# Optimization experiments

Measured on AMD Instinct MI355X. Metric: run time of the kernel, lower is better.

The kernel has to match this reference:

```python
import jax, jax.numpy as jnp
import numpy as np

N = 8388608          # number of samples (2**23)
T_MAX = 100000       # number of distinct time values -> ~84 ties per time


def setup_inputs() -> dict:
    key = jax.random.key(0)
    k1, k2, k3 = jax.random.split(key, 3)
    inp = jax.random.normal(k1, (N,), dtype=jnp.float32)            # log hazards
    target = jax.random.randint(k2, (N,), 0, T_MAX, dtype=jnp.int32)  # times
    weight = jax.random.randint(k3, (N,), 0, 2, dtype=jnp.int32)      # event indicator
    return {"input": inp, "target": target, "weight": weight}


def _cox_efron_npll(log_hz, time, event):
    """Negative Cox partial log-likelihood with Efron tie correction, mean reduction.

    Faithful to torchsurv's _partial_likelihood_efron: per unique time j,
    pll_j = sum_{i in H_j} log_hz_i - sum_{l=0}^{m_j-1} log(D_j - (l/m_j)*T_j)
    where H_j = events at time j, D_j = sum of exp(log_hz) over risk set (t>=t_j),
    T_j = sum of exp(log_hz) over H_j, m_j = |H_j|; loss = -mean over j with m_j>0.
    """
    n = log_hz.shape[0]
    order = jnp.argsort(time)                       # sort by time (group-sum math is tie-order invariant)
    t = time[order]
    lh = log_hz[order]
    ev = event[order].astype(lh.dtype)

    # group id per sample: 0..(num_unique-1), padded groups beyond that are empty
    new_grp = jnp.concatenate([jnp.zeros((1,), jnp.int32), (t[1:] != t[:-1]).astype(jnp.int32)])
    seg = jnp.cumsum(new_grp)                       # [n] int32

    hz = jnp.exp(lh)
    grp_hz = jax.ops.segment_sum(hz, seg, num_segments=n)          # sum exp per time group
    denom_naive = jnp.cumsum(grp_hz[::-1])[::-1]                   # risk-set sums (suffix over groups)
    m = jax.ops.segment_sum(ev, seg, num_segments=n)               # events per group
    log_nom = jax.ops.segment_sum(lh * ev, seg, num_segments=n)    # sum of log_hz over H_j
    ties = jax.ops.segment_sum(hz * ev, seg, num_segments=n)       # sum of exp over H_j

    # rank l in [0, m_j) of each event within its group
    csum_e = jnp.cumsum(ev)
    events_before = jnp.concatenate([jnp.zeros((1,), lh.dtype), jnp.cumsum(m)[:-1]])
    rank = csum_e - 1.0 - events_before[seg]
    mg = jnp.maximum(m[seg], 1.0)
    term = jnp.where(ev > 0.0,
                     jnp.log(denom_naive[seg] - (rank / mg) * ties[seg]),
                     0.0)
    log_denom = jax.ops.segment_sum(term, seg, num_segments=n)

    include = (m > 0.0).astype(lh.dtype)
    pll = jnp.where(m > 0.0, log_nom - log_denom, 0.0)
    # reduction='mean': -pll.nanmean() over groups that contain events
    return -(jnp.sum(pll) / jnp.sum(include))


def reference(input, target, weight):
    return _cox_efron_npll(input, target, weight)
```

## Files before the change

### kernel.cpp

```cpp
#include <hip/hip_runtime.h>

#define TMAXV 100000
#define CHUNK 256
#define NCHUNK ((TMAXV + CHUNK - 1) / CHUNK)
#define WB 256
#define LOGWB 8
#define SB ((TMAXV + WB - 1) / WB)
#define SBP 512
#define TILE 4096
#define RPT 16
#define KS 8
#define CAP 4096
#define RPH (CAP / 256)


__device__ __forceinline__ float block_reduce_sum(float v, float* sdata) {
    int lane = threadIdx.x & 63;
    int wid  = threadIdx.x >> 6;
    #pragma unroll
    for (int off = 32; off > 0; off >>= 1)
        v += __shfl_down(v, off, 64);
    if (lane == 0) sdata[wid] = v;
    __syncthreads();
    if (wid == 0) {
        v = (lane < 4) ? sdata[lane] : 0.0f;
        v += __shfl_down(v, 2, 64);
        v += __shfl_down(v, 1, 64);
    }
    return v;
}


__global__ void count_pfx_kernel(const int* __restrict__ tgt,
                                 int* __restrict__ pfx_arr,
                                 int* __restrict__ cnt_t, int n) {
    __shared__ int lc[SBP];
    __shared__ int ls[SBP];
    int tid = threadIdx.x, tile = blockIdx.x;
    lc[tid] = 0; lc[tid + 256] = 0;
    __syncthreads();
    int lo = tile * TILE, hi = min(n, lo + TILE);
    for (int i = lo + tid; i < hi; i += 256)
        atomicAdd(&lc[tgt[i] >> LOGWB], 1);
    __syncthreads();
    int c0 = lc[tid], c1 = lc[tid + 256];
    int i1 = tid + 256;
    ls[tid] = c0; ls[i1] = c1;
    __syncthreads();
    for (int off = 1; off < SBP; off <<= 1) {
        int a0 = (tid >= off) ? ls[tid - off] : 0;
        int a1 = (i1  >= off) ? ls[i1  - off] : 0;
        __syncthreads();
        ls[tid] += a0; ls[i1] += a1;
        __syncthreads();
    }
    size_t rb = (size_t)tile * SBP;
    pfx_arr[rb + tid] = ls[tid] - c0;
    pfx_arr[rb + i1]  = ls[i1]  - c1;
    cnt_t[rb + tid] = c0;
    cnt_t[rb + i1]  = c1;
}

__global__ void transpose_kernel(const int* __restrict__ A,
                                 int* __restrict__ B, int rows, int cols) {
    __shared__ int tl[32][33];
    int bx = blockIdx.x * 32, by = blockIdx.y * 32;
    int x = threadIdx.x, y = threadIdx.y;
    #pragma unroll
    for (int j = 0; j < 32; j += 8)
        if (by + y + j < rows && bx + x < cols)
            tl[y + j][x] = A[(size_t)(by + y + j) * cols + bx + x];
    __syncthreads();
    #pragma unroll
    for (int j = 0; j < 32; j += 8)
        if (bx + y + j < cols && by + x < rows)
            B[(size_t)(bx + y + j) * rows + by + x] = tl[x][y + j];
}

__global__ void tile_scan_kernel(int* __restrict__ cnt_s,
                                 int* __restrict__ totals, int nt) {
    __shared__ int ls[256];
    int s = blockIdx.x, tid = threadIdx.x;
    int run = 0;
    for (int t0 = 0; t0 < nt; t0 += 256) {
        int t = t0 + tid;
        int c = (t < nt) ? cnt_s[(size_t)s * nt + t] : 0;
        ls[tid] = c;
        __syncthreads();
        for (int off = 1; off < 256; off <<= 1) {
            int a = (tid >= off) ? ls[tid - off] : 0;
            __syncthreads();
            ls[tid] += a;
            __syncthreads();
        }
        int incl = ls[tid];
        int tot  = ls[255];
        if (t < nt) cnt_s[(size_t)s * nt + t] = run + incl - c;
        run += tot;
        __syncthreads();
    }
    if (tid == 0) totals[s] = run;
}

__global__ void bucket_base_kernel(const int* __restrict__ totals,
                                   int* __restrict__ base, int n) {
    __shared__ int ls[SBP];
    int tid = threadIdx.x;
    int c = totals[tid];
    ls[tid] = c;
    __syncthreads();
    for (int off = 1; off < SBP; off <<= 1) {
        int a = (tid >= off) ? ls[tid - off] : 0;
        __syncthreads();
        ls[tid] += a;
        __syncthreads();
    }
    base[tid] = ls[tid] - c;
    if (tid == 0) base[SBP] = n;
}

__global__ void scatter_kernel(const float* __restrict__ lh,
                               const int*   __restrict__ tgt,
                               const int*   __restrict__ ev,
                               const int*   __restrict__ pfx_arr,
                               const int*   __restrict__ tilebase_t,
                               const int*   __restrict__ base,
                               unsigned* __restrict__ val,
                               double* __restrict__ acc, int n) {
    __shared__ uint2 fd[TILE];
    __shared__ int pfx[SBP];
    __shared__ int tb[SBP];
    __shared__ int lrank[SBP];
    __shared__ float sdata[4];
    int tid  = threadIdx.x;
    int tile = blockIdx.x;
    int lo   = tile * TILE;
    int cnt_here = min(TILE, n - lo);
    int i1 = tid + 256;
    size_t rb = (size_t)tile * SBP;

    pfx[tid] = pfx_arr[rb + tid];
    pfx[i1]  = pfx_arr[rb + i1];
    tb[tid]  = base[tid] + tilebase_t[rb + tid];
    tb[i1]   = base[i1]  + tilebase_t[rb + i1];
    lrank[tid] = 0; lrank[i1] = 0;

    unsigned rbits[RPT];
    int      rk[RPT];
    float xl = 0.f;
    if (lo + TILE <= n) {
        const int4*   tgt4 = (const int4*)(tgt + lo);
        const int4*   ev4  = (const int4*)(ev + lo);
        const float4* lh4  = (const float4*)(lh + lo);
        #pragma unroll
        for (int q = 0; q < RPT / 4; ++q) {
            int idx = q * 256 + tid;
            int4   t4 = tgt4[idx];
            int4   e4 = ev4[idx];
            float4 x4 = lh4[idx];
            int   tv[4] = {t4.x, t4.y, t4.z, t4.w};
            int   evv[4] = {e4.x, e4.y, e4.z, e4.w};
            float xv[4] = {x4.x, x4.y, x4.z, x4.w};
            #pragma unroll
            for (int j = 0; j < 4; ++j) {
                int k = q * 4 + j;
                int e = evv[j] & 1;
                float x = xv[j];
                float h = __expf(x);
                rbits[k] = (__float_as_uint(h) & 0x7FFFFF00u)
                         | (unsigned)(tv[j] & (WB - 1))
                         | ((unsigned)e << 31);
                rk[k] = tv[j] >> LOGWB;
                if (e) xl += x;
            }
        }
    } else {
        #pragma unroll
        for (int k = 0; k < RPT; ++k) {
            int i = lo + k * 256 + tid;
            if (i < n) {
                int t = tgt[i];
                int e = ev[i] & 1;
                float x = lh[i];
                float h = __expf(x);
                rbits[k] = (__float_as_uint(h) & 0x7FFFFF00u)
                         | (unsigned)(t & (WB - 1))
                         | ((unsigned)e << 31);
                rk[k] = t >> LOGWB;
                if (e) xl += x;
            } else {
                rk[k] = -1;
            }
        }
    }
    __syncthreads();

    #pragma unroll
    for (int k = 0; k < RPT; ++k) {
        if (rk[k] >= 0) {
            int b = rk[k];
            int r = atomicAdd(&lrank[b], 1);
            fd[pfx[b] + r] = make_uint2(rbits[k], (unsigned)(tb[b] + r));
        }
    }
    __syncthreads();

    for (int p = tid; p < cnt_here; p += 256) {
        uint2 r2 = fd[p];
        val[r2.y] = r2.x;
    }

    float rl = block_reduce_sum(xl, sdata);
    if (tid == 0) atomicAdd(&acc[2], (double)rl);
}

__global__ void bucket_hist_kernel(const unsigned* __restrict__ val,
                                   const int* __restrict__ base,
                                   float* __restrict__ partials,
                                   float* __restrict__ chunk_sum) {
    __shared__ unsigned fv[CAP];
    __shared__ unsigned cnt[WB];
    __shared__ unsigned rankc[WB];
    __shared__ unsigned pfx[WB];
    __shared__ unsigned ls[WB];
    __shared__ float sdata[4];
    int tid = threadIdx.x;
    int b   = blockIdx.x >> 3;
    int k   = blockIdx.x & (KS - 1);
    int lo0 = base[b], len = base[b + 1] - lo0;
    int lo  = lo0 + (int)(((long long)len * k) / KS);
    int hi  = lo0 + (int)(((long long)len * (k + 1)) / KS);

    float sh = 0.f, cm = 0.f, th = 0.f;

    for (int c0 = lo; c0 < hi; c0 += CAP) {
        int c1 = min(hi, c0 + CAP);
        cnt[tid] = 0; rankc[tid] = 0;
        __syncthreads();

        unsigned rv[RPH];
        int      rs[RPH];
        #pragma unroll
        for (int u = 0; u < RPH; ++u) {
            int i = c0 + u * 256 + tid;
            if (i < c1) {
                rv[u] = val[i];
                rs[u] = (int)(rv[u] & (WB - 1));
                atomicAdd(&cnt[rs[u]], 1u);
            } else {
                rs[u] = -1;
            }
        }
        __syncthreads();

        unsigned c = cnt[tid];
        ls[tid] = c;
        __syncthreads();
        for (int off = 1; off < 256; off <<= 1) {
            unsigned a = (tid >= off) ? ls[tid - off] : 0u;
            __syncthreads();
            ls[tid] += a;
            __syncthreads();
        }
        pfx[tid] = ls[tid] - c;
        __syncthreads();

        #pragma unroll
        for (int u = 0; u < RPH; ++u) {
            if (rs[u] >= 0) {
                unsigned r = atomicAdd(&rankc[rs[u]], 1u);
                fv[pfx[rs[u]] + r] = rv[u];
            }
        }
        __syncthreads();

        int s0 = (int)pfx[tid], e0 = s0 + (int)cnt[tid];
        for (int p = s0; p < e0; ++p) {
            unsigned bits = fv[p];
            float h = fabsf(__uint_as_float(bits));
            sh += h;
            if (bits >> 31) { cm += 1.0f; th += h; }
        }
        __syncthreads();
    }

    float* pbase = partials + (size_t)blockIdx.x * 3 * WB;
    pbase[0 * WB + tid] = sh;
    pbase[1 * WB + tid] = cm;
    pbase[2 * WB + tid] = th;

    float st = block_reduce_sum(sh, sdata);
    if (tid == 0) unsafeAtomicAdd(&chunk_sum[b], st);
}

__global__ void chunk_scan_kernel(const float* __restrict__ chunk_sum,
                                  double* __restrict__ chunk_off) {
    __shared__ double ds[512];
    int tid = threadIdx.x;
    double own = (tid < NCHUNK) ? (double)chunk_sum[tid] : 0.0;
    ds[tid] = own;
    __syncthreads();
    for (int off = 1; off < 512; off <<= 1) {
        double add = (tid + off < 512) ? ds[tid + off] : 0.0;
        __syncthreads();
        ds[tid] += add;
        __syncthreads();
    }
    if (tid < NCHUNK) chunk_off[tid] = ds[tid] - own;
}

__global__ void pll_suffix_kernel(const float* __restrict__ partials,
                                  const double* __restrict__ chunk_off,
                                  double* __restrict__ acc) {
    __shared__ float sf[CHUNK];
    __shared__ float sdata[4];
    __shared__ float sdata2[4];
    int tid = threadIdx.x;
    int b   = blockIdx.x;
    float sh = 0.f, cm = 0.f, th = 0.f;
    #pragma unroll
    for (int k = 0; k < KS; ++k) {
        const float* pbase = partials + (size_t)(b * KS + k) * 3 * WB;
        sh += pbase[0 * WB + tid];
        cm += pbase[1 * WB + tid];
        th += pbase[2 * WB + tid];
    }
    sf[tid] = sh;
    __syncthreads();
    for (int off = 1; off < CHUNK; off <<= 1) {
        float add = (tid + off < CHUNK) ? sf[tid + off] : 0.0f;
        __syncthreads();
        sf[tid] += add;
        __syncthreads();
    }
    int t = b * CHUNK + tid;
    float pll = 0.0f, inc = 0.0f;
    if (t < TMAXV && cm > 0.5f) {
        float D    = (float)(chunk_off[b] + (double)sf[tid]);
        int   mi   = (int)(cm + 0.5f);
        float step = th / cm;
        float s = 0.0f;
        for (int l = 0; l < mi; ++l)
            s += __logf(D - (float)l * step);
        pll = -s;
        inc = 1.0f;
    }
    float rp = block_reduce_sum(pll, sdata);
    __syncthreads();
    float ri = block_reduce_sum(inc, sdata2);
    if (threadIdx.x == 0) {
        atomicAdd(&acc[0], (double)rp);
        atomicAdd(&acc[1], (double)ri);
    }
}

__global__ void finalize_kernel(const double* __restrict__ acc,
                                float* __restrict__ out) {
    double cnt = acc[1];
    out[0] = (cnt > 0.0) ? (float)(-(acc[0] + acc[2]) / cnt) : 0.0f;
}

__global__ void hist_kernel(const float* __restrict__ lh,
                            const int*   __restrict__ tgt,
                            const int*   __restrict__ ev,
                            float* __restrict__ sum_hz,
                            float* __restrict__ mcnt,
                            float* __restrict__ log_nom,
                            float* __restrict__ ties,
                            int n) {
    int i = blockIdx.x * blockDim.x + threadIdx.x;
    if (i >= n) return;
    float x = lh[i];
    int   t = tgt[i];
    int   e = ev[i];
    float h = __expf(x);
    unsafeAtomicAdd(&sum_hz[t], h);
    if (e) {
        unsafeAtomicAdd(&mcnt[t], 1.0f);
        unsafeAtomicAdd(&log_nom[t], x);
        unsafeAtomicAdd(&ties[t], h);
    }
}

__global__ void chunk_sum_kernel(const float* __restrict__ sum_hz,
                                 float* __restrict__ chunk_sum) {
    __shared__ float sdata[4];
    int i = blockIdx.x * CHUNK + threadIdx.x;
    float v = (i < TMAXV) ? sum_hz[i] : 0.0f;
    v = block_reduce_sum(v, sdata);
    if (threadIdx.x == 0) chunk_sum[blockIdx.x] = v;
}

__global__ void pll_kernel(const float* __restrict__ mcnt,
                           const float* __restrict__ log_nom,
                           const float* __restrict__ ties,
                           const float* __restrict__ sum_hz,
                           const double* __restrict__ chunk_off,
                           double* __restrict__ acc) {
    __shared__ float sf[CHUNK];
    __shared__ float sdata[4];
    __shared__ float sdata2[4];
    int tid = threadIdx.x;
    int t   = blockIdx.x * CHUNK + tid;
    float v = (t < TMAXV) ? sum_hz[t] : 0.0f;
    sf[tid] = v;
    __syncthreads();
    for (int off = 1; off < CHUNK; off <<= 1) {
        float add = (tid + off < CHUNK) ? sf[tid + off] : 0.0f;
        __syncthreads();
        sf[tid] += add;
        __syncthreads();
    }
    float pll = 0.0f, inc = 0.0f;
    if (t < TMAXV) {
        float mv = mcnt[t];
        if (mv > 0.5f) {
            float D    = (float)(chunk_off[blockIdx.x] + (double)sf[tid]);
            float T    = ties[t];
            int   mi   = (int)(mv + 0.5f);
            float step = T / mv;
            float s = 0.0f;
            for (int l = 0; l < mi; ++l)
                s += __logf(D - (float)l * step);
            pll = log_nom[t] - s;
            inc = 1.0f;
        }
    }
    float rp = block_reduce_sum(pll, sdata);
    __syncthreads();
    float ri = block_reduce_sum(inc, sdata2);
    if (threadIdx.x == 0) {
        atomicAdd(&acc[0], (double)rp);
        atomicAdd(&acc[1], (double)ri);
    }
}

extern "C" void kernel_launch(void* const* d_in, const int* in_sizes, int n_in,
                              void* d_out, int out_size, void* d_ws, size_t ws_size,
                              hipStream_t stream) {
    const float* lh  = (const float*)d_in[0];
    const int*   tgt = (const int*)d_in[1];
    const int*   ev  = (const int*)d_in[2];
    float*       out = (float*)d_out;
    int n  = in_sizes[0];
    int nt = (n + TILE - 1) / TILE;

    char* ws = (char*)d_ws;
    size_t off = 0;
    auto take = [&](size_t bytes, size_t align) {
        off = (off + align - 1) & ~(align - 1);
        size_t r = off; off += bytes; return r;
    };
    size_t o_acc    = take(32, 16);
    size_t o_csum   = take((size_t)SBP * 4, 16);
    size_t zero_bytes = off;
    size_t o_base   = take((size_t)(SBP + 1) * 4, 16);
    size_t o_totals = take((size_t)SBP * 4, 16);
    size_t o_coff   = take((size_t)NCHUNK * 8, 16);
    size_t o_pfx    = take((size_t)nt * SBP * 4, 16);
    size_t o_cntt   = take((size_t)nt * SBP * 4, 16);
    size_t o_cnts   = take((size_t)nt * SBP * 4, 16);
    size_t o_val    = take((size_t)n * 4, 16);
    size_t need     = off;
    size_t part_sz  = (size_t)SB * KS * 3 * WB * 4;
    size_t o_part   = o_pfx;
    if (o_part + part_sz > need) need = o_part + part_sz;

    if (ws_size >= need) {
        double*   acc       = (double*)(ws + o_acc);
        float*    chunk_sum = (float*)(ws + o_csum);
        int*      base      = (int*)(ws + o_base);
        int*      totals    = (int*)(ws + o_totals);
        double*   chunk_off = (double*)(ws + o_coff);
        int*      pfx_arr   = (int*)(ws + o_pfx);
        int*      cnt_t     = (int*)(ws + o_cntt);
        int*      cnt_s     = (int*)(ws + o_cnts);
        unsigned* val       = (unsigned*)(ws + o_val);
        float*    partials  = (float*)(ws + o_part);

        hipMemsetAsync(d_ws, 0, zero_bytes, stream);

        count_pfx_kernel<<<nt, 256, 0, stream>>>(tgt, pfx_arr, cnt_t, n);
        transpose_kernel<<<dim3(SBP / 32, (nt + 31) / 32), dim3(32, 8), 0, stream>>>(
            cnt_t, cnt_s, nt, SBP);
        tile_scan_kernel<<<SBP, 256, 0, stream>>>(cnt_s, totals, nt);
        bucket_base_kernel<<<1, SBP, 0, stream>>>(totals, base, n);
        transpose_kernel<<<dim3((nt + 31) / 32, SBP / 32), dim3(32, 8), 0, stream>>>(
            cnt_s, cnt_t, SBP, nt);
        scatter_kernel<<<nt, 256, 0, stream>>>(lh, tgt, ev, pfx_arr, cnt_t, base, val, acc, n);
        bucket_hist_kernel<<<SB * KS, 256, 0, stream>>>(val, base, partials, chunk_sum);
        chunk_scan_kernel<<<1, 512, 0, stream>>>(chunk_sum, chunk_off);
        pll_suffix_kernel<<<NCHUNK, 256, 0, stream>>>(partials, chunk_off, acc);
        finalize_kernel<<<1, 1, 0, stream>>>(acc, out);
    } else {
        size_t f = 0;
        auto ftake = [&](size_t bytes, size_t align) {
            f = (f + align - 1) & ~(align - 1);
            size_t r = f; f += bytes; return r;
        };
        size_t f_acc  = ftake(32, 16);
        size_t f_sum  = ftake((size_t)TMAXV * 4, 16);
        size_t f_m    = ftake((size_t)TMAXV * 4, 16);
        size_t f_ln   = ftake((size_t)TMAXV * 4, 16);
        size_t f_ties = ftake((size_t)TMAXV * 4, 16);
        size_t zb     = f;
        size_t f_csum = ftake((size_t)NCHUNK * 4, 16);
        size_t f_coff = ftake((size_t)NCHUNK * 8, 8);

        double* acc     = (double*)(ws + f_acc);
        float*  sum_hz  = (float*)(ws + f_sum);
        float*  mcnt    = (float*)(ws + f_m);
        float*  log_nom = (float*)(ws + f_ln);
        float*  ties    = (float*)(ws + f_ties);
        float*  chunk_sum = (float*)(ws + f_csum);
        double* chunk_off = (double*)(ws + f_coff);

        hipMemsetAsync(d_ws, 0, zb, stream);

        hist_kernel<<<(n + 255) / 256, 256, 0, stream>>>(lh, tgt, ev, sum_hz, mcnt, log_nom, ties, n);
        chunk_sum_kernel<<<NCHUNK, 256, 0, stream>>>(sum_hz, chunk_sum);
        chunk_scan_kernel<<<1, 512, 0, stream>>>(chunk_sum, chunk_off);
        pll_kernel<<<NCHUNK, 256, 0, stream>>>(mcnt, log_nom, ties, sum_hz, chunk_off, acc);
        finalize_kernel<<<1, 1, 0, stream>>>(acc, out);
    }
}
```

Measured before the change: 228.6 us.

## Move record encoding into count kernel and shrink scatter shared buffer

The count pass now also computes the packed exp/time/event records, writes them to a workspace array, and accumulates the event log-hazard sum. The scatter pass then reads only the precomputed bits and targets. The scatter's shared staging buffer is split into a 4-byte record plus a 2-byte bucket id, and destinations are recomputed at write time, to cut LDS usage. The trade-off is an extra full-size global write and read of the encoded array, plus a larger workspace requirement; a fallback path keeps the old behaviour when the workspace is too small.

```diff
diff --git a/kernel.cpp b/kernel.cpp
--- a/kernel.cpp
+++ b/kernel.cpp
@@ -30,6 +30,13 @@
     return v;
 }
 
+__device__ __forceinline__ unsigned encode_rec(float x, int t, int e) {
+    float h = __expf(x);
+    return (__float_as_uint(h) & 0x7FFFFF00u)
+         | (unsigned)(t & (WB - 1))
+         | ((unsigned)e << 31);
+}
+
 
 __global__ void count_pfx_kernel(const int* __restrict__ tgt,
                                  int* __restrict__ pfx_arr,
@@ -59,6 +66,75 @@
     pfx_arr[rb + i1]  = ls[i1]  - c1;
     cnt_t[rb + tid] = c0;
     cnt_t[rb + i1]  = c1;
+}
+
+__global__ void count_encode_kernel(const int* __restrict__ tgt,
+                                    const float* __restrict__ lh,
+                                    const int* __restrict__ ev,
+                                    int* __restrict__ pfx_arr,
+                                    int* __restrict__ cnt_t,
+                                    unsigned* __restrict__ bitsArr,
+                                    double* __restrict__ acc, int n) {
+    __shared__ int lc[SBP];
+    __shared__ int ls[SBP];
+    __shared__ float sdata[4];
+    int tid = threadIdx.x, tile = blockIdx.x;
+    lc[tid] = 0; lc[tid + 256] = 0;
+    __syncthreads();
+    int lo = tile * TILE;
+    float xl = 0.f;
+    if (lo + TILE <= n) {
+        const int4*   tgt4 = (const int4*)(tgt + lo);
+        const int4*   ev4  = (const int4*)(ev + lo);
+        const float4* lh4  = (const float4*)(lh + lo);
+        uint4* b4 = (uint4*)(bitsArr + lo);
+        #pragma unroll
+        for (int q = 0; q < RPT / 4; ++q) {
+            int idx = q * 256 + tid;
+            int4   t4 = tgt4[idx];
+            int4   e4 = ev4[idx];
+            float4 x4 = lh4[idx];
+            uint4 o;
+            o.x = encode_rec(x4.x, t4.x, e4.x & 1); if (e4.x & 1) xl += x4.x;
+            o.y = encode_rec(x4.y, t4.y, e4.y & 1); if (e4.y & 1) xl += x4.y;
+            o.z = encode_rec(x4.z, t4.z, e4.z & 1); if (e4.z & 1) xl += x4.z;
+            o.w = encode_rec(x4.w, t4.w, e4.w & 1); if (e4.w & 1) xl += x4.w;
+            b4[idx] = o;
+            atomicAdd(&lc[t4.x >> LOGWB], 1);
+            atomicAdd(&lc[t4.y >> LOGWB], 1);
+            atomicAdd(&lc[t4.z >> LOGWB], 1);
+            atomicAdd(&lc[t4.w >> LOGWB], 1);
+        }
+    } else {
+        int hi = min(n, lo + TILE);
+        for (int i = lo + tid; i < hi; i += 256) {
+            int t = tgt[i];
+            int e = ev[i] & 1;
+            float x = lh[i];
+            bitsArr[i] = encode_rec(x, t, e);
+            if (e) xl += x;
+            atomicAdd(&lc[t >> LOGWB], 1);
+        }
+    }
+    __syncthreads();
+    int c0 = lc[tid], c1 = lc[tid + 256];
+    int i1 = tid + 256;
+    ls[tid] = c0; ls[i1] = c1;
+    __syncthreads();
+    for (int off = 1; off < SBP; off <<= 1) {
+        int a0 = (tid >= off) ? ls[tid - off] : 0;
+        int a1 = (i1  >= off) ? ls[i1  - off] : 0;
+        __syncthreads();
+        ls[tid] += a0; ls[i1] += a1;
+        __syncthreads();
+    }
+    size_t rb = (size_t)tile * SBP;
+    pfx_arr[rb + tid] = ls[tid] - c0;
+    pfx_arr[rb + i1]  = ls[i1]  - c1;
+    cnt_t[rb + tid] = c0;
+    cnt_t[rb + i1]  = c1;
+    float rl = block_reduce_sum(xl, sdata);
+    if (tid == 0) atomicAdd(&acc[2], (double)rl);
 }
 
 __global__ void transpose_kernel(const int* __restrict__ A,
@@ -122,12 +198,14 @@
 __global__ void scatter_kernel(const float* __restrict__ lh,
                                const int*   __restrict__ tgt,
                                const int*   __restrict__ ev,
+                               const unsigned* __restrict__ bitsArr,
                                const int*   __restrict__ pfx_arr,
                                const int*   __restrict__ tilebase_t,
                                const int*   __restrict__ base,
                                unsigned* __restrict__ val,
-                               double* __restrict__ acc, int n) {
-    __shared__ uint2 fd[TILE];
+                               double* __restrict__ acc, int n, int fused) {
+    __shared__ unsigned fu[TILE];
+    __shared__ unsigned short bidv[TILE];
     __shared__ int pfx[SBP];
     __shared__ int tb[SBP];
     __shared__ int lrank[SBP];
@@ -148,48 +226,54 @@
     unsigned rbits[RPT];
     int      rk[RPT];
     float xl = 0.f;
-    if (lo + TILE <= n) {
-        const int4*   tgt4 = (const int4*)(tgt + lo);
-        const int4*   ev4  = (const int4*)(ev + lo);
-        const float4* lh4  = (const float4*)(lh + lo);
-        #pragma unroll
-        for (int q = 0; q < RPT / 4; ++q) {
-            int idx = q * 256 + tid;
-            int4   t4 = tgt4[idx];
-            int4   e4 = ev4[idx];
-            float4 x4 = lh4[idx];
-            int   tv[4] = {t4.x, t4.y, t4.z, t4.w};
-            int   evv[4] = {e4.x, e4.y, e4.z, e4.w};
-            float xv[4] = {x4.x, x4.y, x4.z, x4.w};
+    if (fused) {
+        if (lo + TILE <= n) {
+            const uint4* b4  = (const uint4*)(bitsArr + lo);
+            const int4*  tg4 = (const int4*)(tgt + lo);
             #pragma unroll
-            for (int j = 0; j < 4; ++j) {
-                int k = q * 4 + j;
-                int e = evv[j] & 1;
-                float x = xv[j];
-                float h = __expf(x);
-                rbits[k] = (__float_as_uint(h) & 0x7FFFFF00u)
-                         | (unsigned)(tv[j] & (WB - 1))
-                         | ((unsigned)e << 31);
-                rk[k] = tv[j] >> LOGWB;
-                if (e) xl += x;
+            for (int q = 0; q < RPT / 4; ++q) {
+                int idx = q * 256 + tid;
+                uint4 bb = b4[idx];
+                int4  t4 = tg4[idx];
+                rbits[q*4+0] = bb.x; rk[q*4+0] = t4.x >> LOGWB;
+                rbits[q*4+1] = bb.y; rk[q*4+1] = t4.y >> LOGWB;
+                rbits[q*4+2] = bb.z; rk[q*4+2] = t4.z >> LOGWB;
+                rbits[q*4+3] = bb.w; rk[q*4+3] = t4.w >> LOGWB;
             }
+        } else {
+            #pragma unroll
+            for (int k = 0; k < RPT; ++k) {
+                int i = lo + k * 256 + tid;
+                if (i < n) { rbits[k] = bitsArr[i]; rk[k] = tgt[i] >> LOGWB; }
+                else rk[k] = -1;
+            }
         }
     } else {
-        #pragma unroll
-        for (int k = 0; k < RPT; ++k) {
-            int i = lo + k * 256 + tid;
-            if (i < n) {
-                int t = tgt[i];
-                int e = ev[i] & 1;
-                float x = lh[i];
-                float h = __expf(x);
-                rbits[k] = (__float_as_uint(h) & 0x7FFFFF00u)
-                         | (unsigned)(t & (WB - 1))
-                         | ((unsigned)e << 31);
-                rk[k] = t >> LOGWB;
-                if (e) xl += x;
-            } else {
-                rk[k] = -1;
+        if (lo + TILE <= n) {
+            const int4*   tgt4 = (const int4*)(tgt + lo);
+            const int4*   ev4  = (const int4*)(ev + lo);
+            const float4* lh4  = (const float4*)(lh + lo);
+            #pragma unroll
+            for (int q = 0; q < RPT / 4; ++q) {
+                int idx = q * 256 + tid;
+                int4   t4 = tgt4[idx];
+                int4   e4 = ev4[idx];
+                float4 x4 = lh4[idx];
+                rbits[q*4+0] = encode_rec(x4.x, t4.x, e4.x & 1); rk[q*4+0] = t4.x >> LOGWB; if (e4.x & 1) xl += x4.x;
+                rbits[q*4+1] = encode_rec(x4.y, t4.y, e4.y & 1); rk[q*4+1] = t4.y >> LOGWB; if (e4.y & 1) xl += x4.y;
+                rbits[q*4+2] = encode_rec(x4.z, t4.z, e4.z & 1); rk[q*4+2] = t4.z >> LOGWB; if (e4.z & 1) xl += x4.z;
+                rbits[q*4+3] = encode_rec(x4.w, t4.w, e4.w & 1); rk[q*4+3] = t4.w >> LOGWB; if (e4.w & 1) xl += x4.w;
+            }
+        } else {
+            #pragma unroll
+            for (int k = 0; k < RPT; ++k) {
+                int i = lo + k * 256 + tid;
+                if (i < n) {
+                    int t = tgt[i]; int e = ev[i] & 1; float x = lh[i];
+                    rbits[k] = encode_rec(x, t, e);
+                    rk[k] = t >> LOGWB;
+                    if (e) xl += x;
+                } else rk[k] = -1;
             }
         }
     }
@@ -200,18 +284,35 @@
         if (rk[k] >= 0) {
             int b = rk[k];
             int r = atomicAdd(&lrank[b], 1);
-            fd[pfx[b] + r] = make_uint2(rbits[k], (unsigned)(tb[b] + r));
-        }
-    }
-    __syncthreads();
-
-    for (int p = tid; p < cnt_here; p += 256) {
-        uint2 r2 = fd[p];
-        val[r2.y] = r2.x;
-    }
-
-    float rl = block_reduce_sum(xl, sdata);
-    if (tid == 0) atomicAdd(&acc[2], (double)rl);
+            int pos = pfx[b] + r;
+            fu[pos]   = rbits[k];
+            bidv[pos] = (unsigned short)b;
+        }
+    }
+    __syncthreads();
+
+    int pairs = cnt_here >> 1;
+    const uint2* fu2 = (const uint2*)fu;
+    const unsigned* bid2 = (const unsigned*)bidv;
+    for (int q = tid; q < pairs; q += 256) {
+        uint2 bb = fu2[q];
+        unsigned bp = bid2[q];
+        int b0 = (int)(bp & 0xFFFFu);
+        int b1 = (int)(bp >> 16);
+        int p0 = q * 2;
+        val[tb[b0] + (p0     - pfx[b0])] = bb.x;
+        val[tb[b1] + (p0 + 1 - pfx[b1])] = bb.y;
+    }
+    if ((cnt_here & 1) && tid == 0) {
+        int p = cnt_here - 1;
+        int b = (int)bidv[p];
+        val[tb[b] + (p - pfx[b])] = fu[p];
+    }
+
+    if (!fused) {
+        float rl = block_reduce_sum(xl, sdata);
+        if (tid == 0) atomicAdd(&acc[2], (double)rl);
+    }
 }
 
 __global__ void bucket_hist_kernel(const unsigned* __restrict__ val,
@@ -461,12 +562,16 @@
     size_t o_cntt   = take((size_t)nt * SBP * 4, 16);
     size_t o_cnts   = take((size_t)nt * SBP * 4, 16);
     size_t o_val    = take((size_t)n * 4, 16);
-    size_t need     = off;
+    size_t need_med = off;
+    size_t o_bits   = take((size_t)n * 4, 16);
+    size_t need_pri = off;
     size_t part_sz  = (size_t)SB * KS * 3 * WB * 4;
     size_t o_part   = o_pfx;
-    if (o_part + part_sz > need) need = o_part + part_sz;
-
-    if (ws_size >= need) {
+    if (o_part + part_sz > need_med) need_med = o_part + part_sz;
+    if (o_part + part_sz > need_pri) need_pri = o_part + part_sz;
+
+    if (ws_size >= need_med) {
+        int fused = (ws_size >= need_pri) ? 1 : 0;
         double*   acc       = (double*)(ws + o_acc);
         float*    chunk_sum = (float*)(ws + o_csum);
         int*      base      = (int*)(ws + o_base);
@@ -476,18 +581,23 @@
         int*      cnt_t     = (int*)(ws + o_cntt);
         int*      cnt_s     = (int*)(ws + o_cnts);
         unsigned* val       = (unsigned*)(ws + o_val);
+        unsigned* bitsArr   = (unsigned*)(ws + o_bits);
         float*    partials  = (float*)(ws + o_part);
 
         hipMemsetAsync(d_ws, 0, zero_bytes, stream);
 
-        count_pfx_kernel<<<nt, 256, 0, stream>>>(tgt, pfx_arr, cnt_t, n);
+        if (fused)
+            count_encode_kernel<<<nt, 256, 0, stream>>>(tgt, lh, ev, pfx_arr, cnt_t, bitsArr, acc, n);
+        else
+            count_pfx_kernel<<<nt, 256, 0, stream>>>(tgt, pfx_arr, cnt_t, n);
         transpose_kernel<<<dim3(SBP / 32, (nt + 31) / 32), dim3(32, 8), 0, stream>>>(
             cnt_t, cnt_s, nt, SBP);
         tile_scan_kernel<<<SBP, 256, 0, stream>>>(cnt_s, totals, nt);
         bucket_base_kernel<<<1, SBP, 0, stream>>>(totals, base, n);
         transpose_kernel<<<dim3((nt + 31) / 32, SBP / 32), dim3(32, 8), 0, stream>>>(
             cnt_s, cnt_t, SBP, nt);
-        scatter_kernel<<<nt, 256, 0, stream>>>(lh, tgt, ev, pfx_arr, cnt_t, base, val, acc, n);
+        scatter_kernel<<<nt, 256, 0, stream>>>(lh, tgt, ev, bitsArr, pfx_arr, cnt_t, base,
+                                               val, acc, n, fused);
         bucket_hist_kernel<<<SB * KS, 256, 0, stream>>>(val, base, partials, chunk_sum);
         chunk_scan_kernel<<<1, 512, 0, stream>>>(chunk_sum, chunk_off);
         pll_suffix_kernel<<<NCHUNK, 256, 0, stream>>>(partials, chunk_off, acc);
```

New measurement: 233.0 us. No clear change (+1.9%).

## Drop transpose and chunk-scan kernels, fold scans into consumers, slim scatter staging

Applied to the files above, without the earlier changes.

Removes both transpose launches by having the tile scan read the tile-major count matrix with strided loads, and having the scatter kernel read tile bases strided. It also drops the chunk_scan launch: each pll_suffix block now recomputes its own suffix offset by summing the later chunk sums in double. The scatter kernel stages a 4-byte record plus a 16-bit bucket id instead of an 8-byte pair, recomputing destinations from shared tables. count_pfx gets vectorised int4 loads. The aim is fewer launches and less global traffic, at the cost of uncoalesced strided reads and redundant per-block reduction work.

```diff
diff --git a/kernel.cpp b/kernel.cpp
--- a/kernel.cpp
+++ b/kernel.cpp
@@ -30,6 +30,29 @@
     return v;
 }
 
+__device__ __forceinline__ double block_reduce_sum_d(double v, double* sdata) {
+    int lane = threadIdx.x & 63;
+    int wid  = threadIdx.x >> 6;
+    #pragma unroll
+    for (int off = 32; off > 0; off >>= 1)
+        v += __shfl_down(v, off, 64);
+    if (lane == 0) sdata[wid] = v;
+    __syncthreads();
+    if (wid == 0) {
+        v = (lane < 4) ? sdata[lane] : 0.0;
+        v += __shfl_down(v, 2, 64);
+        v += __shfl_down(v, 1, 64);
+    }
+    return v;
+}
+
+__device__ __forceinline__ unsigned encode_rec(float x, int t, int e) {
+    float h = __expf(x);
+    return (__float_as_uint(h) & 0x7FFFFF00u)
+         | (unsigned)(t & (WB - 1))
+         | ((unsigned)e << 31);
+}
+
 
 __global__ void count_pfx_kernel(const int* __restrict__ tgt,
                                  int* __restrict__ pfx_arr,
@@ -39,9 +62,22 @@
     int tid = threadIdx.x, tile = blockIdx.x;
     lc[tid] = 0; lc[tid + 256] = 0;
     __syncthreads();
-    int lo = tile * TILE, hi = min(n, lo + TILE);
-    for (int i = lo + tid; i < hi; i += 256)
-        atomicAdd(&lc[tgt[i] >> LOGWB], 1);
+    int lo = tile * TILE;
+    if (lo + TILE <= n) {
+        const int4* tgt4 = (const int4*)(tgt + lo);
+        #pragma unroll
+        for (int q = 0; q < RPT / 4; ++q) {
+            int4 t4 = tgt4[q * 256 + tid];
+            atomicAdd(&lc[t4.x >> LOGWB], 1);
+            atomicAdd(&lc[t4.y >> LOGWB], 1);
+            atomicAdd(&lc[t4.z >> LOGWB], 1);
+            atomicAdd(&lc[t4.w >> LOGWB], 1);
+        }
+    } else {
+        int hi = min(n, lo + TILE);
+        for (int i = lo + tid; i < hi; i += 256)
+            atomicAdd(&lc[tgt[i] >> LOGWB], 1);
+    }
     __syncthreads();
     int c0 = lc[tid], c1 = lc[tid + 256];
     int i1 = tid + 256;
@@ -61,30 +97,15 @@
     cnt_t[rb + i1]  = c1;
 }
 
-__global__ void transpose_kernel(const int* __restrict__ A,
-                                 int* __restrict__ B, int rows, int cols) {
-    __shared__ int tl[32][33];
-    int bx = blockIdx.x * 32, by = blockIdx.y * 32;
-    int x = threadIdx.x, y = threadIdx.y;
-    #pragma unroll
-    for (int j = 0; j < 32; j += 8)
-        if (by + y + j < rows && bx + x < cols)
-            tl[y + j][x] = A[(size_t)(by + y + j) * cols + bx + x];
-    __syncthreads();
-    #pragma unroll
-    for (int j = 0; j < 32; j += 8)
-        if (bx + y + j < cols && by + x < rows)
-            B[(size_t)(bx + y + j) * rows + by + x] = tl[x][y + j];
-}
-
-__global__ void tile_scan_kernel(int* __restrict__ cnt_s,
-                                 int* __restrict__ totals, int nt) {
+__global__ void tile_scan_direct_kernel(const int* __restrict__ cnt_t,
+                                        int* __restrict__ tilebase_s,
+                                        int* __restrict__ totals, int nt) {
     __shared__ int ls[256];
     int s = blockIdx.x, tid = threadIdx.x;
     int run = 0;
     for (int t0 = 0; t0 < nt; t0 += 256) {
         int t = t0 + tid;
-        int c = (t < nt) ? cnt_s[(size_t)s * nt + t] : 0;
+        int c = (t < nt) ? cnt_t[(size_t)t * SBP + s] : 0;
         ls[tid] = c;
         __syncthreads();
         for (int off = 1; off < 256; off <<= 1) {
@@ -95,7 +116,7 @@
         }
         int incl = ls[tid];
         int tot  = ls[255];
-        if (t < nt) cnt_s[(size_t)s * nt + t] = run + incl - c;
+        if (t < nt) tilebase_s[(size_t)s * nt + t] = run + incl - c;
         run += tot;
         __syncthreads();
     }
@@ -123,11 +144,12 @@
                                const int*   __restrict__ tgt,
                                const int*   __restrict__ ev,
                                const int*   __restrict__ pfx_arr,
-                               const int*   __restrict__ tilebase_t,
+                               const int*   __restrict__ tilebase_s,
                                const int*   __restrict__ base,
                                unsigned* __restrict__ val,
-                               double* __restrict__ acc, int n) {
-    __shared__ uint2 fd[TILE];
+                               double* __restrict__ acc, int n, int nt) {
+    __shared__ unsigned fu[TILE];
+    __shared__ unsigned short bidv[TILE];
     __shared__ int pfx[SBP];
     __shared__ int tb[SBP];
     __shared__ int lrank[SBP];
@@ -141,8 +163,8 @@
 
     pfx[tid] = pfx_arr[rb + tid];
     pfx[i1]  = pfx_arr[rb + i1];
-    tb[tid]  = base[tid] + tilebase_t[rb + tid];
-    tb[i1]   = base[i1]  + tilebase_t[rb + i1];
+    tb[tid]  = base[tid] + tilebase_s[(size_t)tid * nt + tile];
+    tb[i1]   = base[i1]  + tilebase_s[(size_t)i1  * nt + tile];
     lrank[tid] = 0; lrank[i1] = 0;
 
     unsigned rbits[RPT];
@@ -158,39 +180,21 @@
             int4   t4 = tgt4[idx];
             int4   e4 = ev4[idx];
             float4 x4 = lh4[idx];
-            int   tv[4] = {t4.x, t4.y, t4.z, t4.w};
-            int   evv[4] = {e4.x, e4.y, e4.z, e4.w};
-            float xv[4] = {x4.x, x4.y, x4.z, x4.w};
-            #pragma unroll
-            for (int j = 0; j < 4; ++j) {
-                int k = q * 4 + j;
-                int e = evv[j] & 1;
-                float x = xv[j];
-                float h = __expf(x);
-                rbits[k] = (__float_as_uint(h) & 0x7FFFFF00u)
-                         | (unsigned)(tv[j] & (WB - 1))
-                         | ((unsigned)e << 31);
-                rk[k] = tv[j] >> LOGWB;
-                if (e) xl += x;
-            }
+            rbits[q*4+0] = encode_rec(x4.x, t4.x, e4.x & 1); rk[q*4+0] = t4.x >> LOGWB; if (e4.x & 1) xl += x4.x;
+            rbits[q*4+1] = encode_rec(x4.y, t4.y, e4.y & 1); rk[q*4+1] = t4.y >> LOGWB; if (e4.y & 1) xl += x4.y;
+            rbits[q*4+2] = encode_rec(x4.z, t4.z, e4.z & 1); rk[q*4+2] = t4.z >> LOGWB; if (e4.z & 1) xl += x4.z;
+            rbits[q*4+3] = encode_rec(x4.w, t4.w, e4.w & 1); rk[q*4+3] = t4.w >> LOGWB; if (e4.w & 1) xl += x4.w;
         }
     } else {
         #pragma unroll
         for (int k = 0; k < RPT; ++k) {
             int i = lo + k * 256 + tid;
             if (i < n) {
-                int t = tgt[i];
-                int e = ev[i] & 1;
-                float x = lh[i];
-                float h = __expf(x);
-                rbits[k] = (__float_as_uint(h) & 0x7FFFFF00u)
-                         | (unsigned)(t & (WB - 1))
-                         | ((unsigned)e << 31);
+                int t = tgt[i]; int e = ev[i] & 1; float x = lh[i];
+                rbits[k] = encode_rec(x, t, e);
                 rk[k] = t >> LOGWB;
                 if (e) xl += x;
-            } else {
-                rk[k] = -1;
-            }
+            } else rk[k] = -1;
         }
     }
     __syncthreads();
@@ -200,14 +204,29 @@
         if (rk[k] >= 0) {
             int b = rk[k];
             int r = atomicAdd(&lrank[b], 1);
-            fd[pfx[b] + r] = make_uint2(rbits[k], (unsigned)(tb[b] + r));
-        }
-    }
-    __syncthreads();
-
-    for (int p = tid; p < cnt_here; p += 256) {
-        uint2 r2 = fd[p];
-        val[r2.y] = r2.x;
+            int pos = pfx[b] + r;
+            fu[pos]   = rbits[k];
+            bidv[pos] = (unsigned short)b;
+        }
+    }
+    __syncthreads();
+
+    int pairs = cnt_here >> 1;
+    const uint2* fu2 = (const uint2*)fu;
+    const unsigned* bid2 = (const unsigned*)bidv;
+    for (int q = tid; q < pairs; q += 256) {
+        uint2 bb = fu2[q];
+        unsigned bp = bid2[q];
+        int b0 = (int)(bp & 0xFFFFu);
+        int b1 = (int)(bp >> 16);
+        int p0 = q * 2;
+        val[tb[b0] + (p0     - pfx[b0])] = bb.x;
+        val[tb[b1] + (p0 + 1 - pfx[b1])] = bb.y;
+    }
+    if ((cnt_here & 1) && tid == 0) {
+        int p = cnt_here - 1;
+        int b = (int)bidv[p];
+        val[tb[b] + (p - pfx[b])] = fu[p];
     }
 
     float rl = block_reduce_sum(xl, sdata);
@@ -293,28 +312,14 @@
     if (tid == 0) unsafeAtomicAdd(&chunk_sum[b], st);
 }
 
-__global__ void chunk_scan_kernel(const float* __restrict__ chunk_sum,
-                                  double* __restrict__ chunk_off) {
-    __shared__ double ds[512];
-    int tid = threadIdx.x;
-    double own = (tid < NCHUNK) ? (double)chunk_sum[tid] : 0.0;
-    ds[tid] = own;
-    __syncthreads();
-    for (int off = 1; off < 512; off <<= 1) {
-        double add = (tid + off < 512) ? ds[tid + off] : 0.0;
-        __syncthreads();
-        ds[tid] += add;
-        __syncthreads();
-    }
-    if (tid < NCHUNK) chunk_off[tid] = ds[tid] - own;
-}
-
 __global__ void pll_suffix_kernel(const float* __restrict__ partials,
-                                  const double* __restrict__ chunk_off,
+                                  const float* __restrict__ chunk_sum,
                                   double* __restrict__ acc) {
     __shared__ float sf[CHUNK];
     __shared__ float sdata[4];
     __shared__ float sdata2[4];
+    __shared__ double dsd[4];
+    __shared__ double doff;
     int tid = threadIdx.x;
     int b   = blockIdx.x;
     float sh = 0.f, cm = 0.f, th = 0.f;
@@ -333,10 +338,18 @@
         sf[tid] += add;
         __syncthreads();
     }
+    double mysum = 0.0;
+    for (int j = b + 1 + tid; j < NCHUNK; j += 256)
+        mysum += (double)chunk_sum[j];
+    double red = block_reduce_sum_d(mysum, dsd);
+    if (tid == 0) doff = red;
+    __syncthreads();
+    double off_d = doff;
+
     int t = b * CHUNK + tid;
     float pll = 0.0f, inc = 0.0f;
     if (t < TMAXV && cm > 0.5f) {
-        float D    = (float)(chunk_off[b] + (double)sf[tid]);
+        float D    = (float)(off_d + (double)sf[tid]);
         int   mi   = (int)(cm + 0.5f);
         float step = th / cm;
         float s = 0.0f;
@@ -391,6 +404,22 @@
     if (threadIdx.x == 0) chunk_sum[blockIdx.x] = v;
 }
 
+__global__ void chunk_scan_kernel(const float* __restrict__ chunk_sum,
+                                  double* __restrict__ chunk_off) {
+    __shared__ double ds[512];
+    int tid = threadIdx.x;
+    double own = (tid < NCHUNK) ? (double)chunk_sum[tid] : 0.0;
+    ds[tid] = own;
+    __syncthreads();
+    for (int off = 1; off < 512; off <<= 1) {
+        double add = (tid + off < 512) ? ds[tid + off] : 0.0;
+        __syncthreads();
+        ds[tid] += add;
+        __syncthreads();
+    }
+    if (tid < NCHUNK) chunk_off[tid] = ds[tid] - own;
+}
+
 __global__ void pll_kernel(const float* __restrict__ mcnt,
                            const float* __restrict__ log_nom,
                            const float* __restrict__ ties,
@@ -456,10 +485,9 @@
     size_t zero_bytes = off;
     size_t o_base   = take((size_t)(SBP + 1) * 4, 16);
     size_t o_totals = take((size_t)SBP * 4, 16);
-    size_t o_coff   = take((size_t)NCHUNK * 8, 16);
     size_t o_pfx    = take((size_t)nt * SBP * 4, 16);
     size_t o_cntt   = take((size_t)nt * SBP * 4, 16);
-    size_t o_cnts   = take((size_t)nt * SBP * 4, 16);
+    size_t o_tbs    = take((size_t)nt * SBP * 4, 16);
     size_t o_val    = take((size_t)n * 4, 16);
     size_t need     = off;
     size_t part_sz  = (size_t)SB * KS * 3 * WB * 4;
@@ -471,26 +499,21 @@
         float*    chunk_sum = (float*)(ws + o_csum);
         int*      base      = (int*)(ws + o_base);
         int*      totals    = (int*)(ws + o_totals);
-        double*   chunk_off = (double*)(ws + o_coff);
         int*      pfx_arr   = (int*)(ws + o_pfx);
         int*      cnt_t     = (int*)(ws + o_cntt);
-        int*      cnt_s     = (int*)(ws + o_cnts);
+        int*      tilebase_s= (int*)(ws + o_tbs);
         unsigned* val       = (unsigned*)(ws + o_val);
         float*    partials  = (float*)(ws + o_part);
 
         hipMemsetAsync(d_ws, 0, zero_bytes, stream);
 
         count_pfx_kernel<<<nt, 256, 0, stream>>>(tgt, pfx_arr, cnt_t, n);
-        transpose_kernel<<<dim3(SBP / 32, (nt + 31) / 32), dim3(32, 8), 0, stream>>>(
-            cnt_t, cnt_s, nt, SBP);
-        tile_scan_kernel<<<SBP, 256, 0, stream>>>(cnt_s, totals, nt);
+        tile_scan_direct_kernel<<<SBP, 256, 0, stream>>>(cnt_t, tilebase_s, totals, nt);
         bucket_base_kernel<<<1, SBP, 0, stream>>>(totals, base, n);
-        transpose_kernel<<<dim3((nt + 31) / 32, SBP / 32), dim3(32, 8), 0, stream>>>(
-            cnt_s, cnt_t, SBP, nt);
-        scatter_kernel<<<nt, 256, 0, stream>>>(lh, tgt, ev, pfx_arr, cnt_t, base, val, acc, n);
+        scatter_kernel<<<nt, 256, 0, stream>>>(lh, tgt, ev, pfx_arr, tilebase_s, base,
+                                               val, acc, n, nt);
         bucket_hist_kernel<<<SB * KS, 256, 0, stream>>>(val, base, partials, chunk_sum);
-        chunk_scan_kernel<<<1, 512, 0, stream>>>(chunk_sum, chunk_off);
-        pll_suffix_kernel<<<NCHUNK, 256, 0, stream>>>(partials, chunk_off, acc);
+        pll_suffix_kernel<<<NCHUNK, 256, 0, stream>>>(partials, chunk_sum, acc);
         finalize_kernel<<<1, 1, 0, stream>>>(acc, out);
     } else {
         size_t f = 0;
```

New measurement: 217.9 us. -4.7%, faster.
